# Kernel optimization log

Measured on AMD Instinct MI355X. Metric: run time of the kernel, lower is better.

## Reference

```python
import jax, jax.numpy as jnp
import numpy as np

B, T, C = 2, 2048, 1024
N_HEAD = 16
HEAD_DIM = C // N_HEAD


def setup_inputs() -> dict:
    key = jax.random.key(0)
    k1, k2, k3 = jax.random.split(key, 3)
    x = jax.random.normal(k1, (B, T, C), dtype=jnp.float32)
    # weights stored as [in, out]; torch Linear computes x @ W.T with weight [out, in]
    W_qkv = jax.random.normal(k2, (C, 3 * C), dtype=jnp.float32) * (1.0 / np.sqrt(C))
    W_proj = jax.random.normal(k3, (C, C), dtype=jnp.float32) * (1.0 / np.sqrt(C))
    return {"x": x, "W_qkv": W_qkv, "W_proj": W_proj}


def reference(x, W_qkv, W_proj):
    Bb, Tt, Cc = x.shape
    qkv = x @ W_qkv                                # [B,T,3C]
    q, k, v = jnp.split(qkv, 3, axis=2)
    # [B,T,H,D] -> [B,H,T,D]
    q = q.reshape(Bb, Tt, N_HEAD, HEAD_DIM).transpose(0, 2, 1, 3)
    k = k.reshape(Bb, Tt, N_HEAD, HEAD_DIM).transpose(0, 2, 1, 3)
    v = v.reshape(Bb, Tt, N_HEAD, HEAD_DIM).transpose(0, 2, 1, 3)
    scale = 1.0 / np.sqrt(HEAD_DIM).astype(np.float32)
    att = jnp.einsum('bhqd,bhkd->bhqk', q, k) * scale   # [B,H,T,T]
    causal = jnp.tril(jnp.ones((Tt, Tt), dtype=bool))
    att = jnp.where(causal[None, None], att, -jnp.inf)
    att = jax.nn.softmax(att, axis=-1)
    y = jnp.einsum('bhqk,bhkd->bhqd', att, v)           # [B,H,T,D]
    y = y.transpose(0, 2, 1, 3).reshape(Bb, Tt, Cc)
    return y @ W_proj
```

## Files before the change

### kernel.cpp

```cpp
#include <hip/hip_runtime.h>
#include <hip/hip_bf16.h>
#include <math.h>


typedef __bf16 bf16_t;
typedef __bf16 bf16x4 __attribute__((ext_vector_type(4)));
typedef __bf16 bf16x8 __attribute__((ext_vector_type(8)));
typedef float  f32x4  __attribute__((ext_vector_type(4)));

#define MFMA16(a, b, c) __builtin_amdgcn_mfma_f32_16x16x32_bf16((a), (b), (c), 0, 0, 0)

#define Bn 2
#define Tn 2048
#define Cn 1024
#define Hn 16
#define Dn 64
#define C3 3072
#define Mn 4096
#define QKW 2048
#define NEG_BIG (-1e30f)
#define SCL2 0.18033688011112042f
#define M2   17.31234049066756f

__device__ __forceinline__ void gload_lds16(const void* g, void* l) {
    __builtin_amdgcn_global_load_lds(
        (const __attribute__((address_space(1))) unsigned int*)g,
        (__attribute__((address_space(3))) unsigned int*)l, 16, 0, 0);
}

__global__ __launch_bounds__(256) void transpose_cvt(const float* __restrict__ in,
                                                     bf16_t* __restrict__ out,
                                                     int K, int N) {
    __shared__ float tile[32][33];
    int n0 = blockIdx.x * 32, k0 = blockIdx.y * 32;
    int tx = threadIdx.x, ty = threadIdx.y;
#pragma unroll
    for (int i = 0; i < 32; i += 8)
        tile[ty + i][tx] = in[(size_t)(k0 + ty + i) * N + n0 + tx];
    __syncthreads();
#pragma unroll
    for (int i = 0; i < 32; i += 8)
        out[(size_t)(n0 + ty + i) * K + k0 + tx] = (bf16_t)tile[tx][ty + i];
}

__global__ __launch_bounds__(256) void cvt_bf16(const float* __restrict__ in,
                                                bf16_t* __restrict__ out) {
    size_t i = ((size_t)blockIdx.x * 256 + threadIdx.x) * 8;
    f32x4 a = *(const f32x4*)(in + i);
    f32x4 b = *(const f32x4*)(in + i + 4);
    bf16x8 r;
    r[0] = (bf16_t)a[0]; r[1] = (bf16_t)a[1]; r[2] = (bf16_t)a[2]; r[3] = (bf16_t)a[3];
    r[4] = (bf16_t)b[0]; r[5] = (bf16_t)b[1]; r[6] = (bf16_t)b[2]; r[7] = (bf16_t)b[3];
    *(bf16x8*)(out + i) = r;
}

__global__ __launch_bounds__(256) void gemm_k64(const bf16_t* __restrict__ A, int lda,
                                                const bf16_t* __restrict__ BT, int Kd,
                                                bf16_t* __restrict__ qk,
                                                bf16_t* __restrict__ vT) {
    __shared__ bf16_t As[128 * 64];
    __shared__ bf16_t Bs[128 * 64];

    const int tid = threadIdx.x;
    const int w = tid >> 6, lane = tid & 63;
    const int l16 = lane & 15, quad = lane >> 4;
    const int wm = w & 1, wn = w >> 1;
    const int n0 = blockIdx.x * 128;
    const int m0 = blockIdx.y * 128;

    const int srow = lane >> 3, schk = lane & 7;

    f32x4 zero = {0.f, 0.f, 0.f, 0.f};
    f32x4 acc[4][4];
#pragma unroll
    for (int mb = 0; mb < 4; mb++)
#pragma unroll
        for (int nb = 0; nb < 4; nb++) acc[mb][nb] = zero;

    for (int k = 0; k < Kd; k += 64) {
        __syncthreads();
#pragma unroll
        for (int j = 0; j < 4; j++) {
            int seg = w * 4 + j;
            int r = seg * 8 + srow;
            int cc = schk ^ (r & 7);
            gload_lds16(A + (size_t)(m0 + r) * lda + k + cc * 8, (char*)As + seg * 1024);
            gload_lds16(BT + (size_t)(n0 + r) * Kd + k + cc * 8, (char*)Bs + seg * 1024);
        }
        __syncthreads();

#pragma unroll
        for (int kk = 0; kk < 2; kk++) {
            bf16x8 af[4], bf[4];
#pragma unroll
            for (int mb = 0; mb < 4; mb++) {
                int r = wm * 64 + mb * 16 + l16;
                af[mb] = *(const bf16x8*)((const char*)As + (r * 8 + ((kk * 4 + quad) ^ (r & 7))) * 16);
            }
#pragma unroll
            for (int nb = 0; nb < 4; nb++) {
                int r = wn * 64 + nb * 16 + l16;
                bf[nb] = *(const bf16x8*)((const char*)Bs + (r * 8 + ((kk * 4 + quad) ^ (r & 7))) * 16);
            }
#pragma unroll
            for (int mb = 0; mb < 4; mb++)
#pragma unroll
                for (int nb = 0; nb < 4; nb++)
                    acc[mb][nb] = MFMA16(af[mb], bf[nb], acc[mb][nb]);
        }
    }

#pragma unroll
    for (int mb = 0; mb < 4; mb++)
#pragma unroll
        for (int nb = 0; nb < 4; nb++) {
            const int col = n0 + wn * 64 + nb * 16 + l16;
            const int row0 = m0 + wm * 64 + mb * 16 + quad * 4;
            if (col < 2048) {
#pragma unroll
                for (int rr = 0; rr < 4; rr++)
                    qk[(size_t)(row0 + rr) * QKW + col] = (bf16_t)acc[mb][nb][rr];
            } else {
                int hcol = col - 2048;
                int bb = row0 >> 11, t0 = row0 & 2047;
                bf16x4 pv;
#pragma unroll
                for (int rr = 0; rr < 4; rr++) pv[rr] = (bf16_t)acc[mb][nb][rr];
                *(bf16x4*)(vT + ((size_t)(bb * 1024 + hcol)) * Tn + t0) = pv;
            }
        }
}

template <typename AT, typename CT, int MODE>
__global__ __launch_bounds__(256) void gemm_m97(const AT* __restrict__ A, int lda,
                                                const bf16_t* __restrict__ BT,
                                                CT* __restrict__ Cout, int ldc, int Kd,
                                                bf16_t* __restrict__ qk,
                                                bf16_t* __restrict__ vT) {
    constexpr bool AF32 = (sizeof(AT) == 4);
    __shared__ AT     As[128 * 32];
    __shared__ bf16_t Bs[128 * 32];

    const int tid = threadIdx.x;
    const int w = tid >> 6, lane = tid & 63;
    const int l16 = lane & 15, quad = lane >> 4;
    const int wm = w & 1, wn = w >> 1;
    const int n0 = blockIdx.x * 128;
    const int m0 = blockIdx.y * 128;

    f32x4 zero = {0.f, 0.f, 0.f, 0.f};
    f32x4 acc[4][4];
#pragma unroll
    for (int mb = 0; mb < 4; mb++)
#pragma unroll
        for (int nb = 0; nb < 4; nb++) acc[mb][nb] = zero;

    for (int k = 0; k < Kd; k += 32) {
        __syncthreads();
        if (AF32) {
#pragma unroll
            for (int j = 0; j < 4; j++) {
                int seg = w * 4 + j;
                int r = seg * 8 + (lane >> 3);
                int cc = (lane & 7) ^ (r & 7);
                const float* g = (const float*)A + (size_t)(m0 + r) * lda + k + cc * 4;
                gload_lds16(g, (char*)As + seg * 1024);
            }
        } else {
#pragma unroll
            for (int j = 0; j < 2; j++) {
                int seg = w * 2 + j;
                int r = seg * 16 + (lane >> 2);
                int cc = (lane & 3) ^ (r & 3);
                const bf16_t* g = (const bf16_t*)A + (size_t)(m0 + r) * lda + k + cc * 8;
                gload_lds16(g, (char*)As + seg * 1024);
            }
        }
#pragma unroll
        for (int j = 0; j < 2; j++) {
            int seg = w * 2 + j;
            int r = seg * 16 + (lane >> 2);
            int cc = (lane & 3) ^ (r & 3);
            const bf16_t* g = BT + (size_t)(n0 + r) * Kd + k + cc * 8;
            gload_lds16(g, (char*)Bs + seg * 1024);
        }
        __syncthreads();

        bf16x8 af[4], bf[4];
#pragma unroll
        for (int mb = 0; mb < 4; mb++) {
            int r = wm * 64 + mb * 16 + l16;
            if (AF32) {
                f32x4 x0 = *(const f32x4*)((const char*)As + (r * 8 + ((quad * 2) ^ (r & 7))) * 16);
                f32x4 x1 = *(const f32x4*)((const char*)As + (r * 8 + ((quad * 2 + 1) ^ (r & 7))) * 16);
                bf16x8 t;
                t[0] = (bf16_t)x0[0]; t[1] = (bf16_t)x0[1]; t[2] = (bf16_t)x0[2]; t[3] = (bf16_t)x0[3];
                t[4] = (bf16_t)x1[0]; t[5] = (bf16_t)x1[1]; t[6] = (bf16_t)x1[2]; t[7] = (bf16_t)x1[3];
                af[mb] = t;
            } else {
                af[mb] = *(const bf16x8*)((const char*)As + (r * 4 + (quad ^ (r & 3))) * 16);
            }
        }
#pragma unroll
        for (int nb = 0; nb < 4; nb++) {
            int r = wn * 64 + nb * 16 + l16;
            bf[nb] = *(const bf16x8*)((const char*)Bs + (r * 4 + (quad ^ (r & 3))) * 16);
        }
#pragma unroll
        for (int mb = 0; mb < 4; mb++)
#pragma unroll
            for (int nb = 0; nb < 4; nb++)
                acc[mb][nb] = MFMA16(af[mb], bf[nb], acc[mb][nb]);
    }

#pragma unroll
    for (int mb = 0; mb < 4; mb++)
#pragma unroll
        for (int nb = 0; nb < 4; nb++) {
            const int col = n0 + wn * 64 + nb * 16 + l16;
            const int row0 = m0 + wm * 64 + mb * 16 + quad * 4;
            if (MODE == 0) {
#pragma unroll
                for (int rr = 0; rr < 4; rr++)
                    Cout[(size_t)(row0 + rr) * ldc + col] = (CT)acc[mb][nb][rr];
            } else {
                if (col < 2048) {
#pragma unroll
                    for (int rr = 0; rr < 4; rr++)
                        qk[(size_t)(row0 + rr) * QKW + col] = (bf16_t)acc[mb][nb][rr];
                } else {
                    int hcol = col - 2048;
                    int bb = row0 >> 11, t0 = row0 & 2047;
                    bf16x4 pv;
#pragma unroll
                    for (int rr = 0; rr < 4; rr++) pv[rr] = (bf16_t)acc[mb][nb][rr];
                    *(bf16x4*)(vT + ((size_t)(bb * 1024 + hcol)) * Tn + t0) = pv;
                }
            }
        }
}

__global__ __launch_bounds__(256) void gemm_s(const bf16_t* __restrict__ A, int lda,
                                              const bf16_t* __restrict__ BT,
                                              float* __restrict__ Cout, int ldc, int Kd) {
    __shared__ bf16_t As[64 * 32];
    __shared__ bf16_t Bs[128 * 32];

    const int tid = threadIdx.x;
    const int w = tid >> 6, lane = tid & 63;
    const int l16 = lane & 15, quad = lane >> 4;
    const int wm = w & 1, wn = w >> 1;
    const int n0 = blockIdx.x * 128;
    const int m0 = blockIdx.y * 64;

    f32x4 zero = {0.f, 0.f, 0.f, 0.f};
    f32x4 acc[2][4];
#pragma unroll
    for (int mb = 0; mb < 2; mb++)
#pragma unroll
        for (int nb = 0; nb < 4; nb++) acc[mb][nb] = zero;

    for (int k = 0; k < Kd; k += 32) {
        __syncthreads();
        {
            int r = w * 16 + (lane >> 2);
            int cc = (lane & 3) ^ (r & 3);
            gload_lds16(A + (size_t)(m0 + r) * lda + k + cc * 8, (char*)As + w * 1024);
        }
#pragma unroll
        for (int j = 0; j < 2; j++) {
            int seg = w * 2 + j;
            int r = seg * 16 + (lane >> 2);
            int cc = (lane & 3) ^ (r & 3);
            gload_lds16(BT + (size_t)(n0 + r) * Kd + k + cc * 8, (char*)Bs + seg * 1024);
        }
        __syncthreads();

        bf16x8 af[2], bf[4];
#pragma unroll
        for (int mb = 0; mb < 2; mb++) {
            int r = wm * 32 + mb * 16 + l16;
            af[mb] = *(const bf16x8*)((const char*)As + (r * 4 + (quad ^ (r & 3))) * 16);
        }
#pragma unroll
        for (int nb = 0; nb < 4; nb++) {
            int r = wn * 64 + nb * 16 + l16;
            bf[nb] = *(const bf16x8*)((const char*)Bs + (r * 4 + (quad ^ (r & 3))) * 16);
        }
#pragma unroll
        for (int mb = 0; mb < 2; mb++)
#pragma unroll
            for (int nb = 0; nb < 4; nb++)
                acc[mb][nb] = MFMA16(af[mb], bf[nb], acc[mb][nb]);
    }

#pragma unroll
    for (int mb = 0; mb < 2; mb++)
#pragma unroll
        for (int nb = 0; nb < 4; nb++) {
            const int col = n0 + wn * 64 + nb * 16 + l16;
            const int row0 = m0 + wm * 32 + mb * 16 + quad * 4;
#pragma unroll
            for (int rr = 0; rr < 4; rr++)
                Cout[(size_t)(row0 + rr) * ldc + col] = acc[mb][nb][rr];
        }
}

__global__ __launch_bounds__(128) void attn_kernel(bf16_t* __restrict__ qk,
                                                   const bf16_t* __restrict__ vT) {
    const int id = blockIdx.x;
    const int pair = id >> 1;
    const int bh = pair & 31;
    const int xx = pair >> 5;
    const int qt = (id & 1) ? (31 - xx) : xx;
    const int b = bh >> 4, h = bh & 15;

    const int tid = threadIdx.x;
    const int wave = tid >> 6, lane = tid & 63;
    const int l16 = lane & 15, quad = lane >> 4;

    __shared__ bf16_t Kt[64 * 64];
    __shared__ bf16_t Vt[64 * 64];
    __shared__ bf16_t Pl[2][32][72];

    bf16_t* qbase = qk + (size_t)b * Tn * QKW + h * Dn;
    const bf16_t* kbase = qk + (size_t)b * Tn * QKW + Cn + h * Dn;
    const bf16_t* vbase = vT + (size_t)(b * 1024 + h * Dn) * Tn;

    const int q0 = qt * 64 + wave * 32;

    bf16x8 qf[2][2];
#pragma unroll
    for (int mb = 0; mb < 2; mb++)
#pragma unroll
        for (int ks = 0; ks < 2; ks++)
            qf[mb][ks] = *(const bf16x8*)(qbase + (size_t)(q0 + mb * 16 + l16) * QKW + ks * 32 + quad * 8);

    bf16x8 ones;
#pragma unroll
    for (int j = 0; j < 8; j++) ones[j] = (bf16_t)1.0f;

    f32x4 zero = {0.f, 0.f, 0.f, 0.f};
    f32x4 o[2][4];
    f32x4 ol[2];
#pragma unroll
    for (int mb = 0; mb < 2; mb++) {
#pragma unroll
        for (int i = 0; i < 4; i++) o[mb][i] = zero;
        ol[mb] = zero;
    }

    const int srow = lane >> 3, schk = lane & 7;

    for (int kb = 0; kb <= qt; kb++) {
        const int key0 = kb * 64;
        __syncthreads();
#pragma unroll
        for (int j = 0; j < 4; j++) {
            int seg = wave * 4 + j;
            int r = seg * 8 + srow;
            int cc = schk ^ (r & 7);
            gload_lds16(kbase + (size_t)(key0 + r) * QKW + cc * 8, (char*)Kt + seg * 1024);
            gload_lds16(vbase + (size_t)r * Tn + key0 + cc * 8, (char*)Vt + seg * 1024);
        }
        __syncthreads();

        f32x4 s[2][4];
#pragma unroll
        for (int nbk = 0; nbk < 4; nbk++) {
            int r = nbk * 16 + l16;
            bf16x8 kf0 = *(const bf16x8*)((const char*)Kt + (r * 8 + (quad ^ (r & 7))) * 16);
            bf16x8 kf1 = *(const bf16x8*)((const char*)Kt + (r * 8 + ((4 + quad) ^ (r & 7))) * 16);
#pragma unroll
            for (int mb = 0; mb < 2; mb++) {
                s[mb][nbk] = zero;
                s[mb][nbk] = MFMA16(kf0, qf[mb][0], s[mb][nbk]);
                s[mb][nbk] = MFMA16(kf1, qf[mb][1], s[mb][nbk]);
            }
        }

        if (kb == qt) {
#pragma unroll
            for (int mb = 0; mb < 2; mb++) {
                int q = q0 + mb * 16 + l16;
#pragma unroll
                for (int nbk = 0; nbk < 4; nbk++)
#pragma unroll
                    for (int r = 0; r < 4; r++) {
                        int key = key0 + nbk * 16 + quad * 4 + r;
                        if (key > q) s[mb][nbk][r] = NEG_BIG;
                    }
            }
        }

#pragma unroll
        for (int mb = 0; mb < 2; mb++)
#pragma unroll
            for (int nbk = 0; nbk < 4; nbk++) {
                bf16x4 pk;
#pragma unroll
                for (int r = 0; r < 4; r++)
                    pk[r] = (bf16_t)__builtin_exp2f(__builtin_fmaf(s[mb][nbk][r], SCL2, -M2));
                *(bf16x4*)(&Pl[wave][mb * 16 + l16][nbk * 16 + quad * 4]) = pk;
            }

#pragma unroll
        for (int ks = 0; ks < 2; ks++) {
            bf16x8 pf0 = *(const bf16x8*)(&Pl[wave][l16][ks * 32 + quad * 8]);
            bf16x8 pf1 = *(const bf16x8*)(&Pl[wave][16 + l16][ks * 32 + quad * 8]);
#pragma unroll
            for (int nbd = 0; nbd < 4; nbd++) {
                int r = nbd * 16 + l16;
                bf16x8 vf = *(const bf16x8*)((const char*)Vt + (r * 8 + ((ks * 4 + quad) ^ (r & 7))) * 16);
                o[0][nbd] = MFMA16(pf0, vf, o[0][nbd]);
                o[1][nbd] = MFMA16(pf1, vf, o[1][nbd]);
            }
            ol[0] = MFMA16(pf0, ones, ol[0]);
            ol[1] = MFMA16(pf1, ones, ol[1]);
        }
    }

#pragma unroll
    for (int mb = 0; mb < 2; mb++)
#pragma unroll
        for (int nbd = 0; nbd < 4; nbd++)
#pragma unroll
            for (int r = 0; r < 4; r++) {
                int t = q0 + mb * 16 + quad * 4 + r;
                float val = o[mb][nbd][r] / ol[mb][r];
                qbase[(size_t)t * QKW + nbd * 16 + l16] = (bf16_t)val;
            }
}

extern "C" void kernel_launch(void* const* d_in, const int* in_sizes, int n_in,
                              void* d_out, int out_size, void* d_ws, size_t ws_size,
                              hipStream_t stream) {
    const float* x     = (const float*)d_in[0];
    const float* Wqkv  = (const float*)d_in[1];
    const float* Wproj = (const float*)d_in[2];
    float* out = (float*)d_out;

    bf16_t* qk     = (bf16_t*)d_ws;
    bf16_t* wqkvT  = qk + (size_t)Mn * QKW;
    bf16_t* wprojT = wqkvT + (size_t)C3 * Cn;
    bf16_t* xb     = wprojT + (size_t)Cn * Cn;
    bf16_t* vT     = (bf16_t*)d_out;

    const size_t NEED_XB = ((size_t)Mn * QKW + (size_t)C3 * Cn +
                            (size_t)Cn * Cn + (size_t)Mn * Cn) * sizeof(bf16_t);

    transpose_cvt<<<dim3(C3 / 32, Cn / 32), dim3(32, 8), 0, stream>>>(Wqkv, wqkvT, Cn, C3);
    transpose_cvt<<<dim3(Cn / 32, Cn / 32), dim3(32, 8), 0, stream>>>(Wproj, wprojT, Cn, Cn);

    if (ws_size >= NEED_XB) {
        cvt_bf16<<<dim3((Mn * Cn) / 2048), 256, 0, stream>>>(x, xb);
        gemm_k64<<<dim3(C3 / 128, Mn / 128), 256, 0, stream>>>(xb, Cn, wqkvT, Cn, qk, vT);
    } else {
        gemm_m97<float, bf16_t, 1><<<dim3(C3 / 128, Mn / 128), 256, 0, stream>>>(
            x, Cn, wqkvT, (bf16_t*)nullptr, 0, Cn, qk, vT);
    }
    attn_kernel<<<dim3(1024), 128, 0, stream>>>(qk, vT);
    gemm_s<<<dim3(Cn / 128, Mn / 64), 256, 0, stream>>>(qk, QKW, wprojT, out, Cn, Cn);
}
```

Before: 200.0 us.

## Split long causal attention tiles across two blocks with atomic partial combine

```diff
diff --git a/kernel.cpp b/kernel.cpp
--- a/kernel.cpp
+++ b/kernel.cpp
@@ -54,6 +54,12 @@
     *(bf16x8*)(out + i) = r;
 }
 
+__global__ __launch_bounds__(256) void zero_f32(float* __restrict__ p) {
+    size_t i = (size_t)blockIdx.x * 256 + threadIdx.x;
+    f32x4 z = {0.f, 0.f, 0.f, 0.f};
+    ((f32x4*)p)[i] = z;
+}
+
 __global__ __launch_bounds__(256) void gemm_k64(const bf16_t* __restrict__ A, int lda,
                                                 const bf16_t* __restrict__ BT, int Kd,
                                                 bf16_t* __restrict__ qk,
@@ -306,13 +312,24 @@
         }
 }
 
-__global__ __launch_bounds__(128) void attn_kernel(bf16_t* __restrict__ qk,
-                                                   const bf16_t* __restrict__ vT) {
+__global__ __launch_bounds__(256) void attn_kernel(bf16_t* __restrict__ qk,
+                                                   const bf16_t* __restrict__ vT,
+                                                   float* __restrict__ oScr,
+                                                   float* __restrict__ lScr,
+                                                   int split) {
     const int id = blockIdx.x;
-    const int pair = id >> 1;
-    const int bh = pair & 31;
-    const int xx = pair >> 5;
-    const int qt = (id & 1) ? (31 - xx) : xx;
+    const int bh = id & 31;
+    const int u = id >> 5;
+    int qt, kb0, kb1, part;
+    if (!split || u < 16) {
+        qt = u; kb0 = 0; kb1 = qt + 1; part = 0;
+    } else {
+        int v = u - 16;
+        qt = 16 + (v >> 1);
+        int n = qt + 1, mid = n >> 1;
+        if (v & 1) { kb0 = mid; kb1 = n; } else { kb0 = 0; kb1 = mid; }
+        part = 1;
+    }
     const int b = bh >> 4, h = bh & 15;
 
     const int tid = threadIdx.x;
@@ -321,43 +338,38 @@
 
     __shared__ bf16_t Kt[64 * 64];
     __shared__ bf16_t Vt[64 * 64];
-    __shared__ bf16_t Pl[2][32][72];
+    __shared__ bf16_t Pl[4][16][72];
 
     bf16_t* qbase = qk + (size_t)b * Tn * QKW + h * Dn;
     const bf16_t* kbase = qk + (size_t)b * Tn * QKW + Cn + h * Dn;
     const bf16_t* vbase = vT + (size_t)(b * 1024 + h * Dn) * Tn;
 
-    const int q0 = qt * 64 + wave * 32;
-
-    bf16x8 qf[2][2];
-#pragma unroll
-    for (int mb = 0; mb < 2; mb++)
-#pragma unroll
-        for (int ks = 0; ks < 2; ks++)
-            qf[mb][ks] = *(const bf16x8*)(qbase + (size_t)(q0 + mb * 16 + l16) * QKW + ks * 32 + quad * 8);
+    const int q0 = qt * 64 + wave * 16;
+
+    bf16x8 qf[2];
+#pragma unroll
+    for (int ks = 0; ks < 2; ks++)
+        qf[ks] = *(const bf16x8*)(qbase + (size_t)(q0 + l16) * QKW + ks * 32 + quad * 8);
 
     bf16x8 ones;
 #pragma unroll
     for (int j = 0; j < 8; j++) ones[j] = (bf16_t)1.0f;
 
     f32x4 zero = {0.f, 0.f, 0.f, 0.f};
-    f32x4 o[2][4];
-    f32x4 ol[2];
-#pragma unroll
-    for (int mb = 0; mb < 2; mb++) {
-#pragma unroll
-        for (int i = 0; i < 4; i++) o[mb][i] = zero;
-        ol[mb] = zero;
-    }
+    f32x4 o[4];
+    f32x4 ol;
+#pragma unroll
+    for (int i = 0; i < 4; i++) o[i] = zero;
+    ol = zero;
 
     const int srow = lane >> 3, schk = lane & 7;
 
-    for (int kb = 0; kb <= qt; kb++) {
+    for (int kb = kb0; kb < kb1; kb++) {
         const int key0 = kb * 64;
         __syncthreads();
 #pragma unroll
-        for (int j = 0; j < 4; j++) {
-            int seg = wave * 4 + j;
+        for (int j = 0; j < 2; j++) {
+            int seg = wave * 2 + j;
             int r = seg * 8 + srow;
             int cc = schk ^ (r & 7);
             gload_lds16(kbase + (size_t)(key0 + r) * QKW + cc * 8, (char*)Kt + seg * 1024);
@@ -365,71 +377,97 @@
         }
         __syncthreads();
 
-        f32x4 s[2][4];
+        f32x4 s[4];
 #pragma unroll
         for (int nbk = 0; nbk < 4; nbk++) {
             int r = nbk * 16 + l16;
             bf16x8 kf0 = *(const bf16x8*)((const char*)Kt + (r * 8 + (quad ^ (r & 7))) * 16);
             bf16x8 kf1 = *(const bf16x8*)((const char*)Kt + (r * 8 + ((4 + quad) ^ (r & 7))) * 16);
-#pragma unroll
-            for (int mb = 0; mb < 2; mb++) {
-                s[mb][nbk] = zero;
-                s[mb][nbk] = MFMA16(kf0, qf[mb][0], s[mb][nbk]);
-                s[mb][nbk] = MFMA16(kf1, qf[mb][1], s[mb][nbk]);
-            }
+            s[nbk] = zero;
+            s[nbk] = MFMA16(kf0, qf[0], s[nbk]);
+            s[nbk] = MFMA16(kf1, qf[1], s[nbk]);
         }
 
         if (kb == qt) {
-#pragma unroll
-            for (int mb = 0; mb < 2; mb++) {
-                int q = q0 + mb * 16 + l16;
-#pragma unroll
-                for (int nbk = 0; nbk < 4; nbk++)
-#pragma unroll
-                    for (int r = 0; r < 4; r++) {
-                        int key = key0 + nbk * 16 + quad * 4 + r;
-                        if (key > q) s[mb][nbk][r] = NEG_BIG;
-                    }
-            }
-        }
-
-#pragma unroll
-        for (int mb = 0; mb < 2; mb++)
-#pragma unroll
-            for (int nbk = 0; nbk < 4; nbk++) {
-                bf16x4 pk;
-#pragma unroll
-                for (int r = 0; r < 4; r++)
-                    pk[r] = (bf16_t)__builtin_exp2f(__builtin_fmaf(s[mb][nbk][r], SCL2, -M2));
-                *(bf16x4*)(&Pl[wave][mb * 16 + l16][nbk * 16 + quad * 4]) = pk;
-            }
+            int q = q0 + l16;
+#pragma unroll
+            for (int nbk = 0; nbk < 4; nbk++)
+#pragma unroll
+                for (int r = 0; r < 4; r++) {
+                    int key = key0 + nbk * 16 + quad * 4 + r;
+                    if (key > q) s[nbk][r] = NEG_BIG;
+                }
+        }
+
+#pragma unroll
+        for (int nbk = 0; nbk < 4; nbk++) {
+            bf16x4 pk;
+#pragma unroll
+            for (int r = 0; r < 4; r++)
+                pk[r] = (bf16_t)__builtin_exp2f(__builtin_fmaf(s[nbk][r], SCL2, -M2));
+            *(bf16x4*)(&Pl[wave][l16][nbk * 16 + quad * 4]) = pk;
+        }
 
 #pragma unroll
         for (int ks = 0; ks < 2; ks++) {
-            bf16x8 pf0 = *(const bf16x8*)(&Pl[wave][l16][ks * 32 + quad * 8]);
-            bf16x8 pf1 = *(const bf16x8*)(&Pl[wave][16 + l16][ks * 32 + quad * 8]);
+            bf16x8 pf = *(const bf16x8*)(&Pl[wave][l16][ks * 32 + quad * 8]);
 #pragma unroll
             for (int nbd = 0; nbd < 4; nbd++) {
                 int r = nbd * 16 + l16;
                 bf16x8 vf = *(const bf16x8*)((const char*)Vt + (r * 8 + ((ks * 4 + quad) ^ (r & 7))) * 16);
-                o[0][nbd] = MFMA16(pf0, vf, o[0][nbd]);
-                o[1][nbd] = MFMA16(pf1, vf, o[1][nbd]);
-            }
-            ol[0] = MFMA16(pf0, ones, ol[0]);
-            ol[1] = MFMA16(pf1, ones, ol[1]);
-        }
-    }
-
-#pragma unroll
-    for (int mb = 0; mb < 2; mb++)
+                o[nbd] = MFMA16(pf, vf, o[nbd]);
+            }
+            ol = MFMA16(pf, ones, ol);
+        }
+    }
+
+    if (part == 0) {
 #pragma unroll
         for (int nbd = 0; nbd < 4; nbd++)
 #pragma unroll
             for (int r = 0; r < 4; r++) {
-                int t = q0 + mb * 16 + quad * 4 + r;
-                float val = o[mb][nbd][r] / ol[mb][r];
+                int t = q0 + quad * 4 + r;
+                float val = o[nbd][r] / ol[r];
                 qbase[(size_t)t * QKW + nbd * 16 + l16] = (bf16_t)val;
             }
+    } else {
+        const int tidx = (bh << 4) | (qt - 16);
+        float* obase = oScr + ((size_t)tidx * 64 + wave * 16) * 64;
+#pragma unroll
+        for (int nbd = 0; nbd < 4; nbd++)
+#pragma unroll
+            for (int r = 0; r < 4; r++)
+                atomicAdd(&obase[(size_t)(quad * 4 + r) * 64 + nbd * 16 + l16], o[nbd][r]);
+        if (l16 == 0) {
+#pragma unroll
+            for (int r = 0; r < 4; r++)
+                atomicAdd(&lScr[(size_t)tidx * 64 + wave * 16 + quad * 4 + r], ol[r]);
+        }
+    }
+}
+
+__global__ __launch_bounds__(256) void attn_combine(const float* __restrict__ oScr,
+                                                    const float* __restrict__ lScr,
+                                                    bf16_t* __restrict__ qk) {
+    const int tidx = blockIdx.x;
+    const int bh = tidx >> 4;
+    const int qt = 16 + (tidx & 15);
+    const int b = bh >> 4, h = bh & 15;
+    const int t = threadIdx.x;
+    const int q = t >> 2;
+    const int d0 = (t & 3) * 16;
+
+    const float* op = oScr + ((size_t)tidx * 64 + q) * 64 + d0;
+    float inv = 1.0f / lScr[(size_t)tidx * 64 + q];
+    bf16_t* dst = qk + ((size_t)b * Tn + qt * 64 + q) * QKW + h * Dn + d0;
+
+    bf16x8 r0, r1;
+#pragma unroll
+    for (int j = 0; j < 8; j++) r0[j] = (bf16_t)(op[j] * inv);
+#pragma unroll
+    for (int j = 0; j < 8; j++) r1[j] = (bf16_t)(op[8 + j] * inv);
+    *(bf16x8*)dst = r0;
+    *(bf16x8*)(dst + 8) = r1;
 }
 
 extern "C" void kernel_launch(void* const* d_in, const int* in_sizes, int n_in,
@@ -444,7 +482,9 @@
     bf16_t* wqkvT  = qk + (size_t)Mn * QKW;
     bf16_t* wprojT = wqkvT + (size_t)C3 * Cn;
     bf16_t* xb     = wprojT + (size_t)Cn * Cn;
+    float*  oScr   = (float*)xb;
     bf16_t* vT     = (bf16_t*)d_out;
+    float*  lScr   = (float*)((char*)d_out + (size_t)QKW * Tn * sizeof(bf16_t));
 
     const size_t NEED_XB = ((size_t)Mn * QKW + (size_t)C3 * Cn +
                             (size_t)Cn * Cn + (size_t)Mn * Cn) * sizeof(bf16_t);
@@ -455,10 +495,14 @@
     if (ws_size >= NEED_XB) {
         cvt_bf16<<<dim3((Mn * Cn) / 2048), 256, 0, stream>>>(x, xb);
         gemm_k64<<<dim3(C3 / 128, Mn / 128), 256, 0, stream>>>(xb, Cn, wqkvT, Cn, qk, vT);
+        zero_f32<<<dim3(2048), 256, 0, stream>>>(oScr);
+        zero_f32<<<dim3(32), 256, 0, stream>>>(lScr);
+        attn_kernel<<<dim3(1536), 256, 0, stream>>>(qk, vT, oScr, lScr, 1);
+        attn_combine<<<dim3(512), 256, 0, stream>>>(oScr, lScr, qk);
     } else {
         gemm_m97<float, bf16_t, 1><<<dim3(C3 / 128, Mn / 128), 256, 0, stream>>>(
             x, Cn, wqkvT, (bf16_t*)nullptr, 0, Cn, qk, vT);
-    }
-    attn_kernel<<<dim3(1024), 128, 0, stream>>>(qk, vT);
+        attn_kernel<<<dim3(1024), 256, 0, stream>>>(qk, vT, nullptr, nullptr, 0);
+    }
     gemm_s<<<dim3(Cn / 128, Mn / 64), 256, 0, stream>>>(qk, QKW, wprojT, out, Cn, Cn);
 }
```

Result: no change. 200.9 us (+0.4%).
